# Kernel optimization log

Measured on AMD Instinct MI355X. Metric: run time of the kernel, lower is better.

The kernel has to match this reference:

```python
import jax, jax.numpy as jnp
import numpy as np

EPS = 1e-6
HEADS = 8


def _block_weights(gh, gw):
    # block centers at (i+0.5, j+0.5); 'cos' transform, column-normalized (sum over dim 0)
    ii, jj = np.meshgrid(np.arange(gh) + 0.5, np.arange(gw) + 0.5, indexing='ij')
    centers = np.stack([ii.ravel(), jj.ravel()], axis=-1)  # [N, 2]
    d = np.linalg.norm(centers[:, None, :] - centers[None, :, :], axis=-1)  # [N, N]
    mat = np.cos(d / d.max() * np.pi / 4.0)
    mat = mat / mat.sum(axis=0, keepdims=True)
    return jnp.asarray(mat, dtype=jnp.float32)


def setup_inputs() -> dict:
    key = jax.random.key(0)
    ks = jax.random.split(key, 5)
    B, N, W, C = 8, 256, 49, 512
    s = 1.0 / np.sqrt(C)
    return {
        'x': jax.random.normal(ks[0], (B, N, W, C), jnp.float32),
        'ln_g': jnp.ones((C,), jnp.float32),
        'ln_b': jnp.zeros((C,), jnp.float32),
        'w_qkv': jax.random.normal(ks[1], (3 * C, C), jnp.float32) * s,  # Linear(dim, 3*dim, bias=False)
        'lepe_w': jax.random.normal(ks[2], (C, 1, 5, 5), jnp.float32) * 0.2,  # depthwise 5x5
        'lepe_b': jnp.zeros((C,), jnp.float32),
        'w_out': jax.random.normal(ks[3], (C, C), jnp.float32) * s,
        'b_out': jnp.zeros((C,), jnp.float32),
    }


def reference(x, ln_g, ln_b, w_qkv, lepe_w, lepe_b, w_out, b_out):
    B, N, Wn, C = x.shape
    H = HEADS
    D = C // H
    gh = gw = int(round(N ** 0.5))   # grid of window blocks
    wh = ww = int(round(Wn ** 0.5))  # tokens per window side

    # LayerNorm over channel dim (torch eps=1e-5, biased var)
    mu = x.mean(-1, keepdims=True)
    var = x.var(-1, keepdims=True)
    xn = (x - mu) / jnp.sqrt(var + 1e-5) * ln_g + ln_b

    # qkv projection
    qkv = jnp.einsum('bnwc,oc->bnwo', xn, w_qkv)
    q, k, v = jnp.split(qkv, 3, axis=-1)  # each [B, N, W, C]

    # LePE: fold v to image [B, C, gh*wh, gw*ww], depthwise conv 5x5 pad 2, unfold back
    img = v.reshape(B, gh, gw, wh, ww, C).transpose(0, 5, 1, 3, 2, 4).reshape(B, C, gh * wh, gw * ww)
    lepe = jax.lax.conv_general_dilated(
        img, lepe_w, window_strides=(1, 1), padding=((2, 2), (2, 2)),
        dimension_numbers=('NCHW', 'OIHW', 'NCHW'), feature_group_count=C)
    lepe = lepe + lepe_b[None, :, None, None]
    lepe = lepe.reshape(B, C, gh, wh, gw, ww).transpose(0, 2, 4, 3, 5, 1).reshape(B, N, Wn, C)

    # ReLU + eps feature maps (qk_norm=False -> identity norms)
    q = jax.nn.relu(q) + EPS
    k = jax.nn.relu(k) + EPS

    # split heads: [B, H, N, W, D]
    def split_heads(t):
        return t.reshape(B, N, Wn, H, D).transpose(0, 3, 1, 2, 4)
    q, k, v = split_heads(q), split_heads(k), split_heads(v)

    # per-block k^T v state: [B, H, N, D, D]
    kv = jnp.einsum('bhnwd,bhnwe->bhnde', k, v)
    weight = _block_weights(gh, gw)  # [N, N]
    kv = jnp.einsum('ij,bhjde->bhide', weight, kv)

    k_sum = k.sum(axis=-2)  # [B, H, N, D]
    qk_sum = jnp.einsum('bhnwd,bhnd->bhnw', q, k_sum)[..., None]  # [B, H, N, W, 1]
    normalizer = jnp.einsum('ij,bhjwo->bhiwo', weight, qk_sum) + EPS

    out = jnp.einsum('bhnwd,bhnde->bhnwe', q, kv) / normalizer  # [B, H, N, W, D]
    out = out.transpose(0, 2, 3, 1, 4).reshape(B, N, Wn, C)
    out = out + lepe
    return jnp.einsum('bnwc,oc->bnwo', out, w_out) + b_out
```

## Files before the change

### kernel.cpp

```cpp
#include <hip/hip_runtime.h>
#include <cstdint>

typedef unsigned short u16;
typedef unsigned int   u32;
typedef u16   u16x8 __attribute__((ext_vector_type(8)));
typedef u16   u16x4 __attribute__((ext_vector_type(4)));
typedef float f32x4 __attribute__((ext_vector_type(4)));
typedef __bf16 bf16x8 __attribute__((ext_vector_type(8)));

#define NB    256
#define WTOK  49
#define CH    512
#define HEADS 8
#define DH    64
#define TOK   100352
#define CO    1536

__device__ __forceinline__ u16 f2bf(float f) {
  u32 u = __float_as_uint(f);
  u = (u + 0x7FFFu + ((u >> 16) & 1u)) >> 16;
  return (u16)u;
}
__device__ __forceinline__ float bf2f(u16 u) { return __uint_as_float(((u32)u) << 16); }

__device__ __forceinline__ void load_lds16(const void* g, void* l) {
  __builtin_amdgcn_global_load_lds(
      reinterpret_cast<__attribute__((address_space(1))) void*>(reinterpret_cast<uintptr_t>(g)),
      reinterpret_cast<__attribute__((address_space(3))) void*>(reinterpret_cast<uintptr_t>(l)),
      16, 0, 0);
}

__global__ void cvt_f32_bf16(const float* __restrict__ in, u16* __restrict__ out, int n8) {
  int i = blockIdx.x * 256 + threadIdx.x;
  if (i < n8) {
    f32x4 a = *(const f32x4*)(in + (long)i * 8);
    f32x4 b = *(const f32x4*)(in + (long)i * 8 + 4);
    u16x8 o;
    o[0]=f2bf(a[0]); o[1]=f2bf(a[1]); o[2]=f2bf(a[2]); o[3]=f2bf(a[3]);
    o[4]=f2bf(b[0]); o[5]=f2bf(b[1]); o[6]=f2bf(b[2]); o[7]=f2bf(b[3]);
    *(u16x8*)(out + (long)i * 8) = o;
  }
}

__global__ void prep_wle(const float* __restrict__ lepe_w, float* __restrict__ wle) {
  int i = blockIdx.x * 256 + threadIdx.x;
  if (i < 12800) {
    int c = i / 25, kk = i % 25;
    wle[kk * 512 + c] = lepe_w[i];
  }
}

__global__ void weight_kernel(u16* __restrict__ Wbf, float* __restrict__ Wt) {
  int j = blockIdx.x, i = threadIdx.x;
  float iy = (float)(i >> 4) + 0.5f, ix = (float)(i & 15) + 0.5f;
  float jy = (float)(j >> 4) + 0.5f, jx = (float)(j & 15) + 0.5f;
  float dy = iy - jy, dx = ix - jx;
  float d = sqrtf(dy * dy + dx * dx);
  const float dmax = 21.213203435596427f;
  float m = cosf(d * (0.78539816339744831f / dmax));
  __shared__ float red[256];
  red[i] = m;
  __syncthreads();
  for (int s = 128; s > 0; s >>= 1) {
    if (i < s) red[i] += red[i + s];
    __syncthreads();
  }
  float w = m / red[0];
  Wbf[i * 256 + j] = f2bf(w);
  Wt[j * 256 + i] = w;
}

__global__ __launch_bounds__(256) void ln_kernel(const float* __restrict__ x,
                                                 const float* __restrict__ g,
                                                 const float* __restrict__ bta,
                                                 u16* __restrict__ xn) {
  int wave = threadIdx.x >> 6, lane = threadIdx.x & 63;
  long t = (long)blockIdx.x * 4 + wave;
  const float* xp = x + t * CH + lane * 8;
  f32x4 a = *(const f32x4*)xp;
  f32x4 b = *(const f32x4*)(xp + 4);
  float s  = a[0]+a[1]+a[2]+a[3]+b[0]+b[1]+b[2]+b[3];
  float sq = a[0]*a[0]+a[1]*a[1]+a[2]*a[2]+a[3]*a[3]+b[0]*b[0]+b[1]*b[1]+b[2]*b[2]+b[3]*b[3];
  for (int m = 1; m < 64; m <<= 1) { s += __shfl_xor(s, m); sq += __shfl_xor(sq, m); }
  float mu = s * (1.0f / 512.0f);
  float var = sq * (1.0f / 512.0f) - mu * mu;
  float rstd = rsqrtf(var + 1e-5f);
  const float* gp = g + lane * 8;
  const float* bp = bta + lane * 8;
  f32x4 g0 = *(const f32x4*)gp, g1 = *(const f32x4*)(gp + 4);
  f32x4 b0 = *(const f32x4*)bp, b1 = *(const f32x4*)(bp + 4);
  u16x8 o;
  o[0] = f2bf((a[0]-mu)*rstd*g0[0] + b0[0]);
  o[1] = f2bf((a[1]-mu)*rstd*g0[1] + b0[1]);
  o[2] = f2bf((a[2]-mu)*rstd*g0[2] + b0[2]);
  o[3] = f2bf((a[3]-mu)*rstd*g0[3] + b0[3]);
  o[4] = f2bf((b[0]-mu)*rstd*g1[0] + b1[0]);
  o[5] = f2bf((b[1]-mu)*rstd*g1[1] + b1[1]);
  o[6] = f2bf((b[2]-mu)*rstd*g1[2] + b1[2]);
  o[7] = f2bf((b[3]-mu)*rstd*g1[3] + b1[3]);
  *(u16x8*)(xn + t * CH + lane * 8) = o;
}

template <int KT>
__device__ __forceinline__ void kstepD(char* sm, const u16* sA, const u16* sB,
                                       int t, int lane_off, int wm, int wn,
                                       f32x4 (&acc)[4][4]) {
  if constexpr (KT + 1 < 16) {
    char* d = sm + ((KT + 1) & 1) * 24576 + t * 16;
    load_lds16(sA + (KT + 1) * 32, d);
    load_lds16(sA + 128 * 512 + (KT + 1) * 32, d + 8192);
    load_lds16(sB + (KT + 1) * 32, d + 16384);
  }
  const char* base = sm + (KT & 1) * 24576 + lane_off;
  bf16x8 fa[4], fb[4];
#pragma unroll
  for (int m = 0; m < 4; m++) fa[m] = *(const bf16x8*)(base + (wm * 4 + m) * 1024);
#pragma unroll
  for (int n = 0; n < 4; n++) fb[n] = *(const bf16x8*)(base + 16384 + (wn * 4 + n) * 1024);
  __builtin_amdgcn_s_setprio(1);
#pragma unroll
  for (int m = 0; m < 4; m++)
#pragma unroll
    for (int n = 0; n < 4; n++)
      acc[m][n] = __builtin_amdgcn_mfma_f32_16x16x32_bf16(fa[m], fb[n], acc[m][n], 0, 0, 0);
  __builtin_amdgcn_s_setprio(0);
  if constexpr (KT + 1 < 16) __syncthreads();
}

template <int EPI>
__global__ __launch_bounds__(512, 4)
void gemmD(const u16* __restrict__ A, const u16* __restrict__ B,
           void* __restrict__ C, const float* __restrict__ bias, int N, int nbn) {
  __shared__ __align__(16) char sm[49152];
  const int nwg = gridDim.x, bid = blockIdx.x;
  const int cpx = nwg >> 3;
  const int vid = (bid & 7) * cpx + (bid >> 3);
  const int bn = vid % nbn, bm = vid / nbn;
  const int t = threadIdx.x, lane = t & 63, wave = t >> 6;
  const int wm = wave >> 1, wn = wave & 1;
  const int fr = lane & 15, fq = lane >> 4;
  const int lane_off = (fr >> 1) * 128 + ((((fr & 1) << 2) + fq) ^ (fr >> 1)) * 16;
  const int sl = (t & 7) ^ ((t >> 3) & 7);
  const u16* sA = A + ((long)bm * 256 + ((t >> 3) << 1) + (sl >> 2)) * 512 + (sl & 3) * 8;
  const u16* sB = B + ((long)bn * 128 + ((t >> 3) << 1) + (sl >> 2)) * 512 + (sl & 3) * 8;
  f32x4 acc[4][4] = {};
  {
    char* d = sm + t * 16;
    load_lds16(sA, d);
    load_lds16(sA + 128 * 512, d + 8192);
    load_lds16(sB, d + 16384);
  }
  __syncthreads();
  kstepD<0>(sm, sA, sB, t, lane_off, wm, wn, acc);
  kstepD<1>(sm, sA, sB, t, lane_off, wm, wn, acc);
  kstepD<2>(sm, sA, sB, t, lane_off, wm, wn, acc);
  kstepD<3>(sm, sA, sB, t, lane_off, wm, wn, acc);
  kstepD<4>(sm, sA, sB, t, lane_off, wm, wn, acc);
  kstepD<5>(sm, sA, sB, t, lane_off, wm, wn, acc);
  kstepD<6>(sm, sA, sB, t, lane_off, wm, wn, acc);
  kstepD<7>(sm, sA, sB, t, lane_off, wm, wn, acc);
  kstepD<8>(sm, sA, sB, t, lane_off, wm, wn, acc);
  kstepD<9>(sm, sA, sB, t, lane_off, wm, wn, acc);
  kstepD<10>(sm, sA, sB, t, lane_off, wm, wn, acc);
  kstepD<11>(sm, sA, sB, t, lane_off, wm, wn, acc);
  kstepD<12>(sm, sA, sB, t, lane_off, wm, wn, acc);
  kstepD<13>(sm, sA, sB, t, lane_off, wm, wn, acc);
  kstepD<14>(sm, sA, sB, t, lane_off, wm, wn, acc);
  kstepD<15>(sm, sA, sB, t, lane_off, wm, wn, acc);
  __syncthreads();
  {
    float* ep = (float*)sm + wave * 1088;
    const long r0 = (long)bm * 256 + wm * 64;
    const int c0 = bn * 128 + wn * 64;
    const int rrow = lane >> 2;
    const int cb = (lane & 3) * 16;
#pragma unroll
    for (int m = 0; m < 4; m++) {
#pragma unroll
      for (int n = 0; n < 4; n++) {
        int c = c0 + n * 16 + fr;
        float badd = (EPI == 2) ? bias[c] : 0.0f;
#pragma unroll
        for (int jj = 0; jj < 4; jj++) {
          float v = acc[m][n][jj];
          if (EPI == 1) { if (c < 1024) v = fmaxf(v, 0.0f) + 1e-6f; }
          if (EPI == 2) v += badd;
          ep[(fq * 4 + jj) * 68 + n * 16 + fr] = v;
        }
      }
      f32x4 rr[4];
#pragma unroll
      for (int i = 0; i < 4; i++)
        rr[i] = *(const f32x4*)&ep[rrow * 68 + cb + i * 4];
      long gr = r0 + m * 16 + rrow;
      if (EPI == 2) {
        float* gp = (float*)C + gr * N + c0 + cb;
#pragma unroll
        for (int i = 0; i < 4; i++) *(f32x4*)(gp + i * 4) = rr[i];
      } else {
        u16x8 o0, o1;
#pragma unroll
        for (int i = 0; i < 4; i++) {
          o0[i] = f2bf(rr[0][i]); o0[4 + i] = f2bf(rr[1][i]);
          o1[i] = f2bf(rr[2][i]); o1[4 + i] = f2bf(rr[3][i]);
        }
        u16* gp = (u16*)C + gr * N + c0 + cb;
        *(u16x8*)gp = o0;
        *(u16x8*)(gp + 8) = o1;
      }
    }
  }
}

template <int EPI>
__global__ __launch_bounds__(256)
void gemm_bt(const u16* __restrict__ A, const u16* __restrict__ B,
             void* __restrict__ C, const float* __restrict__ bias,
             int M, int N, int K, long sAb, long sBb, long sCb) {
  __shared__ u16 As[128 * 32];
  __shared__ u16 Bs[128 * 32];
  const int tid = threadIdx.x;
  const int lane = tid & 63;
  const int wave = tid >> 6;
  const int fr = lane & 15, fq = lane >> 4;
  const int wr = (wave >> 1) * 64, wc = (wave & 1) * 64;
  const long bm = blockIdx.y, bn = blockIdx.x, bz = blockIdx.z;
  const u16* Ab = A + bz * sAb + bm * 128 * (long)K;
  const u16* Bb = B + bz * sBb + bn * 128 * (long)K;
  const int srow = tid >> 2;
  const int scol = (tid & 3) * 8;
  f32x4 acc[4][4] = {};
  for (int k0 = 0; k0 < K; k0 += 32) {
    load_lds16(Ab + (long)srow * K + k0 + scol, As + tid * 8);
    load_lds16(Ab + (long)(srow + 64) * K + k0 + scol, As + 2048 + tid * 8);
    load_lds16(Bb + (long)srow * K + k0 + scol, Bs + tid * 8);
    load_lds16(Bb + (long)(srow + 64) * K + k0 + scol, Bs + 2048 + tid * 8);
    __syncthreads();
    bf16x8 af[4], bf[4];
#pragma unroll
    for (int m = 0; m < 4; m++) af[m] = *(const bf16x8*)&As[(wr + m * 16 + fr) * 32 + fq * 8];
#pragma unroll
    for (int n = 0; n < 4; n++) bf[n] = *(const bf16x8*)&Bs[(wc + n * 16 + fr) * 32 + fq * 8];
#pragma unroll
    for (int m = 0; m < 4; m++)
#pragma unroll
      for (int n = 0; n < 4; n++)
        acc[m][n] = __builtin_amdgcn_mfma_f32_16x16x32_bf16(af[m], bf[n], acc[m][n], 0, 0, 0);
    __syncthreads();
  }
#pragma unroll
  for (int m = 0; m < 4; m++) {
    int r0 = wr + m * 16 + fq * 4;
#pragma unroll
    for (int n = 0; n < 4; n++) {
      int c = (int)bn * 128 + wc + n * 16 + fr;
#pragma unroll
      for (int jj = 0; jj < 4; jj++) {
        long r = bm * 128 + r0 + jj;
        float v = acc[m][n][jj];
        if (EPI == 1) { if (c < 1024) v = fmaxf(v, 0.0f) + 1e-6f; }
        if (EPI == 2) {
          ((float*)C)[bz * sCb + r * N + c] = v + bias[c];
        } else {
          ((u16*)C)[bz * sCb + r * N + c] = f2bf(v);
        }
      }
    }
  }
}

__global__ __launch_bounds__(256)
void fold_v(const u16* __restrict__ qkv, u16* __restrict__ vimg) {
  long i = (long)blockIdx.x * 256 + threadIdx.x;
  int tok = (int)(i >> 6);
  int c0 = ((int)i & 63) * 8;
  int w = tok % WTOK, n = tok / WTOK;
  int b = n >> 8, blk = n & 255;
  int gi = blk >> 4, gj = blk & 15;
  int wi = w / 7, wj = w - wi * 7;
  int y = gi * 7 + wi + 2, x = gj * 7 + wj + 2;
  u16x8 v = *(const u16x8*)(qkv + (long)tok * CO + 1024 + c0);
  *(u16x8*)(vimg + (((long)(b * 116 + y)) * 116 + x) * 512 + c0) = v;
}

__global__ __launch_bounds__(256)
void zero_border(u16* __restrict__ vimg) {
  int y = blockIdx.x, b = blockIdx.y;
  int tid = threadIdx.x;
  u16* row = vimg + ((long)(b * 116 + y)) * 116 * 512;
  u16x8 z = {};
  if (y < 2 || y >= 114) {
    for (int i = tid; i < 116 * 512 / 8; i += 256) *(u16x8*)(row + i * 8) = z;
  } else {
    int col = tid >> 6;
    int x = (col < 2) ? col : 112 + col;
    *(u16x8*)(row + x * 512 + (tid & 63) * 8) = z;
  }
}

__global__ __launch_bounds__(256, 2)
void lepe_conv3(const u16* __restrict__ vimg, const float* __restrict__ wle,
                const float* __restrict__ lb, u16* __restrict__ lepe) {
  const int tid = threadIdx.x;
  const int c0 = (tid & 127) * 4;
  const int x  = blockIdx.x * 2 + (tid >> 7);
  const int ys = blockIdx.y * 14;
  const int b  = blockIdx.z;
  f32x4 wv[25];
#pragma unroll
  for (int k = 0; k < 25; k++) wv[k] = *(const f32x4*)(wle + k * 512 + c0);
  const f32x4 bias = *(const f32x4*)(lb + c0);
  const u16* rbase = vimg + (((long)(b * 116 + ys)) * 116 + x) * 512 + c0;
  u16x4 win[5][5];
#pragma unroll
  for (int j = 0; j < 4; j++) {
    const u16* rp = rbase + (long)j * (116 * 512);
#pragma unroll
    for (int kx = 0; kx < 5; kx++) win[j][kx] = *(const u16x4*)(rp + kx * 512);
  }
  const int gj = x / 7, wj = x - gj * 7;
  u16* ob = lepe + (((long)(b * 256 + blockIdx.y * 32 + gj)) * 49 + wj) * 512 + c0;
#pragma unroll
  for (int i = 0; i < 14; i++) {
    {
      const u16* rp = rbase + (long)(i + 4) * (116 * 512);
#pragma unroll
      for (int kx = 0; kx < 5; kx++) win[(i + 4) % 5][kx] = *(const u16x4*)(rp + kx * 512);
    }
    f32x4 acc = bias;
#pragma unroll
    for (int s = 0; s < 5; s++)
#pragma unroll
      for (int kx = 0; kx < 5; kx++) {
        u16x4 v = win[(i + s) % 5][kx];
        f32x4 w = wv[s * 5 + kx];
#pragma unroll
        for (int c = 0; c < 4; c++) acc[c] += bf2f(v[c]) * w[c];
      }
    u16x4 o;
#pragma unroll
    for (int c = 0; c < 4; c++) o[c] = f2bf(acc[c]);
    *(u16x4*)(ob + ((i / 7) * 784 + (i % 7) * 7) * 512) = o;
  }
}

__global__ __launch_bounds__(256)
void kv_local_kernel(const u16* __restrict__ qkv, u16* __restrict__ KVl,
                     float* __restrict__ qk_sum) {
  int n = blockIdx.x, h = blockIdx.y, b = blockIdx.z;
  int bh = b * HEADS + h;
  long tbase = ((long)(b * NB + n)) * WTOK;
  __shared__ u16 kT[64 * 72];
  __shared__ u16 vT[64 * 72];
  __shared__ u16 qs[49 * 72];
  __shared__ float ksum[64];
  __shared__ float qkp[256];
  int tid = threadIdx.x;
  for (int i = tid; i < (64 * 72) / 2; i += 256) {
    ((u32*)kT)[i] = 0;
    ((u32*)vT)[i] = 0;
  }
  __syncthreads();
  {
    int w = tid >> 3, d0 = (tid & 7) * 8;
    u16x8 k8 = *(const u16x8*)(qkv + (tbase + w) * CO + 512 + h * 64 + d0);
    u16x8 v8 = *(const u16x8*)(qkv + (tbase + w) * CO + 1024 + h * 64 + d0);
#pragma unroll
    for (int i = 0; i < 8; i++) { kT[(d0 + i) * 72 + w] = k8[i]; vT[(d0 + i) * 72 + w] = v8[i]; }
    int w2 = w + 32;
    if (w2 < WTOK) {
      u16x8 k82 = *(const u16x8*)(qkv + (tbase + w2) * CO + 512 + h * 64 + d0);
      u16x8 v82 = *(const u16x8*)(qkv + (tbase + w2) * CO + 1024 + h * 64 + d0);
#pragma unroll
      for (int i = 0; i < 8; i++) { kT[(d0 + i) * 72 + w2] = k82[i]; vT[(d0 + i) * 72 + w2] = v82[i]; }
    }
    if (tid < 196) {
      int wq = tid >> 2, dq = (tid & 3) * 16;
      u16x8 q0 = *(const u16x8*)(qkv + (tbase + wq) * CO + h * 64 + dq);
      u16x8 q1 = *(const u16x8*)(qkv + (tbase + wq) * CO + h * 64 + dq + 8);
      *(u16x8*)&qs[wq * 72 + dq] = q0;
      *(u16x8*)&qs[wq * 72 + dq + 8] = q1;
    }
  }
  __syncthreads();
  if (tid < 64) {
    float s = 0.0f;
#pragma unroll
    for (int c = 0; c < 9; c++) {
      u16x8 r = *(const u16x8*)&kT[tid * 72 + c * 8];
#pragma unroll
      for (int i = 0; i < 8; i++) s += bf2f(r[i]);
    }
    ksum[tid] = s;
  }
  __syncthreads();
  if (tid < 196) {
    int w = tid >> 2, d0 = (tid & 3) * 16;
    float s = 0.0f;
#pragma unroll
    for (int i = 0; i < 16; i++) s += bf2f(qs[w * 72 + d0 + i]) * ksum[d0 + i];
    qkp[tid] = s;
  }
  __syncthreads();
  if (tid < WTOK) {
    float s = qkp[tid * 4] + qkp[tid * 4 + 1] + qkp[tid * 4 + 2] + qkp[tid * 4 + 3];
    qk_sum[((long)bh * NB + n) * WTOK + tid] = s;
  }
  int lane = tid & 63, wave = tid >> 6;
  int fr = lane & 15, fq = lane >> 4;
  f32x4 acc[4] = {};
#pragma unroll
  for (int ks = 0; ks < 2; ks++) {
    bf16x8 a = *(const bf16x8*)&kT[(wave * 16 + fr) * 72 + ks * 32 + fq * 8];
#pragma unroll
    for (int n4 = 0; n4 < 4; n4++) {
      bf16x8 bb = *(const bf16x8*)&vT[(n4 * 16 + fr) * 72 + ks * 32 + fq * 8];
      acc[n4] = __builtin_amdgcn_mfma_f32_16x16x32_bf16(a, bb, acc[n4], 0, 0, 0);
    }
  }
  long obase = ((long)bh * NB + n) * 4096;
#pragma unroll
  for (int n4 = 0; n4 < 4; n4++)
#pragma unroll
    for (int jj = 0; jj < 4; jj++) {
      int d = wave * 16 + fq * 4 + jj;
      int e = n4 * 16 + fr;
      KVl[obase + d * 64 + e] = f2bf(acc[n4][jj]);
    }
}

__global__ __launch_bounds__(256)
void transpose_kv(const u16* __restrict__ in, u16* __restrict__ out) {
  int dt = blockIdx.x, jt = blockIdx.y, bh = blockIdx.z;
  __shared__ u16 t[64 * 72];
  int tid = threadIdx.x;
  {
    int jr = tid >> 2, c0 = (tid & 3) * 16;
    const u16* ip = in + ((long)bh * NB + jt * 64 + jr) * 4096 + dt * 64 + c0;
    *(u16x8*)&t[jr * 72 + c0] = *(const u16x8*)ip;
    *(u16x8*)&t[jr * 72 + c0 + 8] = *(const u16x8*)(ip + 8);
  }
  __syncthreads();
  {
    int der = tid >> 2, j0 = (tid & 3) * 16;
    u16x8 o0, o1;
#pragma unroll
    for (int i = 0; i < 8; i++) o0[i] = t[(j0 + i) * 72 + der];
#pragma unroll
    for (int i = 0; i < 8; i++) o1[i] = t[(j0 + 8 + i) * 72 + der];
    u16* op = out + ((long)bh * 4096 + dt * 64 + der) * 256 + jt * 64 + j0;
    *(u16x8*)op = o0;
    *(u16x8*)(op + 8) = o1;
  }
}

__global__ __launch_bounds__(256)
void norm_kernel(const float* __restrict__ Wt, const float* __restrict__ qk_sum,
                 float* __restrict__ inv_norm) {
  int bh = blockIdx.x, tid = threadIdx.x;
  __shared__ float qk[NB * WTOK];
  for (int i = tid; i < NB * WTOK; i += 256) qk[i] = qk_sum[(long)bh * NB * WTOK + i];
  __syncthreads();
  float acc[WTOK];
#pragma unroll
  for (int w = 0; w < WTOK; w++) acc[w] = 0.0f;
  for (int j = 0; j < NB; j++) {
    float wv = Wt[j * NB + tid];
#pragma unroll
    for (int w = 0; w < WTOK; w++) acc[w] += wv * qk[j * WTOK + w];
  }
  long ob = ((long)bh * NB + tid) * WTOK;
#pragma unroll
  for (int w = 0; w < WTOK; w++) inv_norm[ob + w] = 1.0f / (acc[w] + 1e-6f);
}

__global__ __launch_bounds__(256)
void attn_out_kernel(const u16* __restrict__ qkv, const u16* __restrict__ kvm,
                     const float* __restrict__ inv_norm, const u16* __restrict__ lepe,
                     u16* __restrict__ ebuf) {
  int n = blockIdx.x, h = blockIdx.y, b = blockIdx.z;
  int bh = b * HEADS + h;
  long tbase = ((long)(b * NB + n)) * WTOK;
  __shared__ u16 qs[64 * 72];
  __shared__ u16 kvT[64 * 72];
  __shared__ float inv[WTOK];
  int tid = threadIdx.x;
  if (tid < 196) {
    int w = tid >> 2, d0 = (tid & 3) * 16;
    u16x8 q0 = *(const u16x8*)(qkv + (tbase + w) * CO + h * 64 + d0);
    u16x8 q1 = *(const u16x8*)(qkv + (tbase + w) * CO + h * 64 + d0 + 8);
    *(u16x8*)&qs[w * 72 + d0] = q0;
    *(u16x8*)&qs[w * 72 + d0 + 8] = q1;
  }
  {
    int d = tid >> 2, e0 = (tid & 3) * 16;
    const u16* kp = kvm + ((long)bh * NB + n) * 4096 + d * 64 + e0;
    u16x8 k0 = *(const u16x8*)kp;
    u16x8 k1 = *(const u16x8*)(kp + 8);
#pragma unroll
    for (int i = 0; i < 8; i++) { kvT[(e0 + i) * 72 + d] = k0[i]; kvT[(e0 + 8 + i) * 72 + d] = k1[i]; }
  }
  if (tid < WTOK) inv[tid] = inv_norm[((long)bh * NB + n) * WTOK + tid];
  __syncthreads();
  int lane = tid & 63, wave = tid >> 6;
  int fr = lane & 15, fq = lane >> 4;
  f32x4 acc[4] = {};
#pragma unroll
  for (int ks = 0; ks < 2; ks++) {
    bf16x8 a = *(const bf16x8*)&qs[(wave * 16 + fr) * 72 + ks * 32 + fq * 8];
#pragma unroll
    for (int n4 = 0; n4 < 4; n4++) {
      bf16x8 bb = *(const bf16x8*)&kvT[(n4 * 16 + fr) * 72 + ks * 32 + fq * 8];
      acc[n4] = __builtin_amdgcn_mfma_f32_16x16x32_bf16(a, bb, acc[n4], 0, 0, 0);
    }
  }
#pragma unroll
  for (int n4 = 0; n4 < 4; n4++)
#pragma unroll
    for (int jj = 0; jj < 4; jj++) {
      int w = wave * 16 + fq * 4 + jj;
      if (w < WTOK) {
        int e = n4 * 16 + fr;
        long off = (tbase + w) * CH + h * 64 + e;
        float v = acc[n4][jj] * inv[w] + bf2f(lepe[off]);
        ebuf[off] = f2bf(v);
      }
    }
}

static const size_t OFF_XN    = 0;
static const size_t OFF_QKV   = 102760448;
static const size_t OFF_KVL   = OFF_QKV + 308281344;
static const size_t OFF_KVT   = OFF_KVL + 134217728;
static const size_t OFF_QKS   = OFF_KVT + 134217728;
static const size_t OFF_INV   = OFF_QKS + 3211264;
static const size_t OFF_WBF   = OFF_INV + 3211264;
static const size_t OFF_WTF   = OFF_WBF + 131072;
static const size_t OFF_WQKVB = OFF_WTF + 262144;
static const size_t OFF_WOUTB = OFF_WQKVB + 1572864;
static const size_t OFF_WLE   = OFF_WOUTB + 524288;

extern "C" void kernel_launch(void* const* d_in, const int* in_sizes, int n_in,
                              void* d_out, int out_size, void* d_ws, size_t ws_size,
                              hipStream_t stream) {
  const float* x      = (const float*)d_in[0];
  const float* ln_g   = (const float*)d_in[1];
  const float* ln_b   = (const float*)d_in[2];
  const float* w_qkv  = (const float*)d_in[3];
  const float* lepe_w = (const float*)d_in[4];
  const float* lepe_b = (const float*)d_in[5];
  const float* w_out  = (const float*)d_in[6];
  const float* b_out  = (const float*)d_in[7];
  float* out = (float*)d_out;
  char* ws = (char*)d_ws;

  u16*   xn     = (u16*)(ws + OFF_XN);
  u16*   lepe   = (u16*)(ws + OFF_XN);
  u16*   qkv    = (u16*)(ws + OFF_QKV);
  u16*   KVl    = (u16*)(ws + OFF_KVL);
  u16*   kvm    = (u16*)(ws + OFF_KVL);
  u16*   vimg   = (u16*)(ws + OFF_KVT);
  u16*   KVT    = (u16*)(ws + OFF_KVT);
  u16*   ebuf   = (u16*)(ws + OFF_KVT);
  float* qks    = (float*)(ws + OFF_QKS);
  float* invn   = (float*)(ws + OFF_INV);
  u16*   Wbf    = (u16*)(ws + OFF_WBF);
  float* Wt     = (float*)(ws + OFF_WTF);
  u16*   wqkvb  = (u16*)(ws + OFF_WQKVB);
  u16*   woutb  = (u16*)(ws + OFF_WOUTB);
  float* wle    = (float*)(ws + OFF_WLE);

  cvt_f32_bf16<<<384, 256, 0, stream>>>(w_qkv, wqkvb, 98304);
  cvt_f32_bf16<<<128, 256, 0, stream>>>(w_out, woutb, 32768);
  prep_wle<<<50, 256, 0, stream>>>(lepe_w, wle);
  weight_kernel<<<256, 256, 0, stream>>>(Wbf, Wt);
  zero_border<<<dim3(116, 8), 256, 0, stream>>>(vimg);

  ln_kernel<<<25088, 256, 0, stream>>>(x, ln_g, ln_b, xn);

  gemmD<1><<<4704, 512, 0, stream>>>(xn, wqkvb, (void*)qkv, nullptr, CO, 12);

  fold_v<<<25088, 256, 0, stream>>>(qkv, vimg);
  lepe_conv3<<<dim3(56, 8, 8), 256, 0, stream>>>(vimg, wle, lepe_b, lepe);

  kv_local_kernel<<<dim3(NB, HEADS, 8), 256, 0, stream>>>(qkv, KVl, qks);

  transpose_kv<<<dim3(64, 4, 64), 256, 0, stream>>>(KVl, KVT);

  gemm_bt<0><<<dim3(32, 2, 64), 256, 0, stream>>>(Wbf, KVT, (void*)kvm, nullptr,
                                                  NB, 4096, NB,
                                                  0, (long)4096 * 256, (long)256 * 4096);

  norm_kernel<<<64, 256, 0, stream>>>(Wt, qks, invn);

  attn_out_kernel<<<dim3(NB, HEADS, 8), 256, 0, stream>>>(qkv, kvm, invn, lepe, ebuf);

  gemmD<2><<<1568, 512, 0, stream>>>(ebuf, woutb, (void*)out, b_out, CH, 4);
}
```

Measured before the change: 936.2 us.

## Fuse V fold into QKV GEMM epilogue and compute two conv columns per thread

The QKV GEMM epilogue now writes the V columns straight into the padded image layout instead of a full qkv buffer, and the separate fold_v kernel is removed. kv_local reads V from that image, q/k are stored with a 1024 stride, and ebuf moves to a region that no longer overlaps vimg. The depthwise LePE conv now computes two adjacent x outputs per thread, reusing the overlapping window loads with half as many blocks. This removes one full read/write pass over V and some redundant conv loads, at the cost of scattered epilogue stores and more registers in the conv.

Measured after the change: 891.4 us. -4.8%, faster.

```diff
diff --git a/kernel.cpp b/kernel.cpp
--- a/kernel.cpp
+++ b/kernel.cpp
@@ -14,7 +14,6 @@
 #define HEADS 8
 #define DH    64
 #define TOK   100352
-#define CO    1536
 
 __device__ __forceinline__ u16 f2bf(float f) {
   u32 u = __float_as_uint(f);
@@ -130,7 +129,8 @@
 template <int EPI>
 __global__ __launch_bounds__(512, 4)
 void gemmD(const u16* __restrict__ A, const u16* __restrict__ B,
-           void* __restrict__ C, const float* __restrict__ bias, int N, int nbn) {
+           void* __restrict__ C, u16* __restrict__ vimg,
+           const float* __restrict__ bias, int ldc, int nbn) {
   __shared__ __align__(16) char sm[49152];
   const int nwg = gridDim.x, bid = blockIdx.x;
   const int cpx = nwg >> 3;
@@ -174,6 +174,7 @@
     const int c0 = bn * 128 + wn * 64;
     const int rrow = lane >> 2;
     const int cb = (lane & 3) * 16;
+    const int cc = c0 + cb;
 #pragma unroll
     for (int m = 0; m < 4; m++) {
 #pragma unroll
@@ -194,7 +195,7 @@
         rr[i] = *(const f32x4*)&ep[rrow * 68 + cb + i * 4];
       long gr = r0 + m * 16 + rrow;
       if (EPI == 2) {
-        float* gp = (float*)C + gr * N + c0 + cb;
+        float* gp = (float*)C + gr * ldc + cc;
 #pragma unroll
         for (int i = 0; i < 4; i++) *(f32x4*)(gp + i * 4) = rr[i];
       } else {
@@ -204,7 +205,20 @@
           o0[i] = f2bf(rr[0][i]); o0[4 + i] = f2bf(rr[1][i]);
           o1[i] = f2bf(rr[2][i]); o1[4 + i] = f2bf(rr[3][i]);
         }
-        u16* gp = (u16*)C + gr * N + c0 + cb;
+        u16* gp;
+        if (cc < 1024) {
+          gp = (u16*)C + gr * ldc + cc;
+        } else {
+          int tok = (int)gr;
+          int b2 = tok / 12544;
+          int rem = tok - b2 * 12544;
+          int nn = rem / 49;
+          int w = rem - nn * 49;
+          int wi = w / 7, wj = w - wi * 7;
+          int y = (nn >> 4) * 7 + wi + 2;
+          int xx = (nn & 15) * 7 + wj + 2;
+          gp = vimg + (((long)(b2 * 116 + y)) * 116 + xx) * 512 + (cc - 1024);
+        }
         *(u16x8*)gp = o0;
         *(u16x8*)(gp + 8) = o1;
       }
@@ -270,20 +284,6 @@
 }
 
 __global__ __launch_bounds__(256)
-void fold_v(const u16* __restrict__ qkv, u16* __restrict__ vimg) {
-  long i = (long)blockIdx.x * 256 + threadIdx.x;
-  int tok = (int)(i >> 6);
-  int c0 = ((int)i & 63) * 8;
-  int w = tok % WTOK, n = tok / WTOK;
-  int b = n >> 8, blk = n & 255;
-  int gi = blk >> 4, gj = blk & 15;
-  int wi = w / 7, wj = w - wi * 7;
-  int y = gi * 7 + wi + 2, x = gj * 7 + wj + 2;
-  u16x8 v = *(const u16x8*)(qkv + (long)tok * CO + 1024 + c0);
-  *(u16x8*)(vimg + (((long)(b * 116 + y)) * 116 + x) * 512 + c0) = v;
-}
-
-__global__ __launch_bounds__(256)
 void zero_border(u16* __restrict__ vimg) {
   int y = blockIdx.x, b = blockIdx.y;
   int tid = threadIdx.x;
@@ -299,57 +299,66 @@
 }
 
 __global__ __launch_bounds__(256, 2)
-void lepe_conv3(const u16* __restrict__ vimg, const float* __restrict__ wle,
+void lepe_conv4(const u16* __restrict__ vimg, const float* __restrict__ wle,
                 const float* __restrict__ lb, u16* __restrict__ lepe) {
   const int tid = threadIdx.x;
   const int c0 = (tid & 127) * 4;
-  const int x  = blockIdx.x * 2 + (tid >> 7);
+  const int x0 = blockIdx.x * 4 + (tid >> 7) * 2;
   const int ys = blockIdx.y * 14;
   const int b  = blockIdx.z;
   f32x4 wv[25];
 #pragma unroll
   for (int k = 0; k < 25; k++) wv[k] = *(const f32x4*)(wle + k * 512 + c0);
   const f32x4 bias = *(const f32x4*)(lb + c0);
-  const u16* rbase = vimg + (((long)(b * 116 + ys)) * 116 + x) * 512 + c0;
-  u16x4 win[5][5];
+  const u16* rbase = vimg + (((long)(b * 116 + ys)) * 116 + x0) * 512 + c0;
+  u16x4 win[5][6];
 #pragma unroll
   for (int j = 0; j < 4; j++) {
     const u16* rp = rbase + (long)j * (116 * 512);
 #pragma unroll
-    for (int kx = 0; kx < 5; kx++) win[j][kx] = *(const u16x4*)(rp + kx * 512);
-  }
-  const int gj = x / 7, wj = x - gj * 7;
-  u16* ob = lepe + (((long)(b * 256 + blockIdx.y * 32 + gj)) * 49 + wj) * 512 + c0;
+    for (int kx = 0; kx < 6; kx++) win[j][kx] = *(const u16x4*)(rp + kx * 512);
+  }
+  const int gj0 = x0 / 7, wj0 = x0 - gj0 * 7;
+  const int gj1 = (x0 + 1) / 7, wj1 = (x0 + 1) - gj1 * 7;
+  u16* ob0 = lepe + (((long)(b * 256 + blockIdx.y * 32 + gj0)) * 49 + wj0) * 512 + c0;
+  u16* ob1 = lepe + (((long)(b * 256 + blockIdx.y * 32 + gj1)) * 49 + wj1) * 512 + c0;
 #pragma unroll
   for (int i = 0; i < 14; i++) {
     {
       const u16* rp = rbase + (long)(i + 4) * (116 * 512);
 #pragma unroll
-      for (int kx = 0; kx < 5; kx++) win[(i + 4) % 5][kx] = *(const u16x4*)(rp + kx * 512);
-    }
-    f32x4 acc = bias;
+      for (int kx = 0; kx < 6; kx++) win[(i + 4) % 5][kx] = *(const u16x4*)(rp + kx * 512);
+    }
+    f32x4 a0 = bias, a1 = bias;
 #pragma unroll
     for (int s = 0; s < 5; s++)
 #pragma unroll
       for (int kx = 0; kx < 5; kx++) {
-        u16x4 v = win[(i + s) % 5][kx];
+        u16x4 v0 = win[(i + s) % 5][kx];
+        u16x4 v1 = win[(i + s) % 5][kx + 1];
         f32x4 w = wv[s * 5 + kx];
 #pragma unroll
-        for (int c = 0; c < 4; c++) acc[c] += bf2f(v[c]) * w[c];
+        for (int c = 0; c < 4; c++) {
+          a0[c] += bf2f(v0[c]) * w[c];
+          a1[c] += bf2f(v1[c]) * w[c];
+        }
       }
-    u16x4 o;
-#pragma unroll
-    for (int c = 0; c < 4; c++) o[c] = f2bf(acc[c]);
-    *(u16x4*)(ob + ((i / 7) * 784 + (i % 7) * 7) * 512) = o;
+    u16x4 o0, o1;
+#pragma unroll
+    for (int c = 0; c < 4; c++) { o0[c] = f2bf(a0[c]); o1[c] = f2bf(a1[c]); }
+    long so = (long)((i / 7) * 784 + (i % 7) * 7) * 512;
+    *(u16x4*)(ob0 + so) = o0;
+    *(u16x4*)(ob1 + so) = o1;
   }
 }
 
 __global__ __launch_bounds__(256)
-void kv_local_kernel(const u16* __restrict__ qkv, u16* __restrict__ KVl,
-                     float* __restrict__ qk_sum) {
+void kv_local_kernel(const u16* __restrict__ qk, const u16* __restrict__ vimg,
+                     u16* __restrict__ KVl, float* __restrict__ qk_sum) {
   int n = blockIdx.x, h = blockIdx.y, b = blockIdx.z;
   int bh = b * HEADS + h;
   long tbase = ((long)(b * NB + n)) * WTOK;
+  const int gi = n >> 4, gj = n & 15;
   __shared__ u16 kT[64 * 72];
   __shared__ u16 vT[64 * 72];
   __shared__ u16 qs[49 * 72];
@@ -363,21 +372,25 @@
   __syncthreads();
   {
     int w = tid >> 3, d0 = (tid & 7) * 8;
-    u16x8 k8 = *(const u16x8*)(qkv + (tbase + w) * CO + 512 + h * 64 + d0);
-    u16x8 v8 = *(const u16x8*)(qkv + (tbase + w) * CO + 1024 + h * 64 + d0);
+    u16x8 k8 = *(const u16x8*)(qk + (tbase + w) * 1024 + 512 + h * 64 + d0);
+    int wi = w / 7, wj = w - wi * 7;
+    long va = (((long)(b * 116 + gi * 7 + wi + 2)) * 116 + (gj * 7 + wj + 2)) * 512 + h * 64 + d0;
+    u16x8 v8 = *(const u16x8*)(vimg + va);
 #pragma unroll
     for (int i = 0; i < 8; i++) { kT[(d0 + i) * 72 + w] = k8[i]; vT[(d0 + i) * 72 + w] = v8[i]; }
     int w2 = w + 32;
     if (w2 < WTOK) {
-      u16x8 k82 = *(const u16x8*)(qkv + (tbase + w2) * CO + 512 + h * 64 + d0);
-      u16x8 v82 = *(const u16x8*)(qkv + (tbase + w2) * CO + 1024 + h * 64 + d0);
+      u16x8 k82 = *(const u16x8*)(qk + (tbase + w2) * 1024 + 512 + h * 64 + d0);
+      int wi2 = w2 / 7, wj2 = w2 - wi2 * 7;
+      long va2 = (((long)(b * 116 + gi * 7 + wi2 + 2)) * 116 + (gj * 7 + wj2 + 2)) * 512 + h * 64 + d0;
+      u16x8 v82 = *(const u16x8*)(vimg + va2);
 #pragma unroll
       for (int i = 0; i < 8; i++) { kT[(d0 + i) * 72 + w2] = k82[i]; vT[(d0 + i) * 72 + w2] = v82[i]; }
     }
     if (tid < 196) {
       int wq = tid >> 2, dq = (tid & 3) * 16;
-      u16x8 q0 = *(const u16x8*)(qkv + (tbase + wq) * CO + h * 64 + dq);
-      u16x8 q1 = *(const u16x8*)(qkv + (tbase + wq) * CO + h * 64 + dq + 8);
+      u16x8 q0 = *(const u16x8*)(qk + (tbase + wq) * 1024 + h * 64 + dq);
+      u16x8 q1 = *(const u16x8*)(qk + (tbase + wq) * 1024 + h * 64 + dq + 8);
       *(u16x8*)&qs[wq * 72 + dq] = q0;
       *(u16x8*)&qs[wq * 72 + dq + 8] = q1;
     }
@@ -475,7 +488,7 @@
 }
 
 __global__ __launch_bounds__(256)
-void attn_out_kernel(const u16* __restrict__ qkv, const u16* __restrict__ kvm,
+void attn_out_kernel(const u16* __restrict__ qk, const u16* __restrict__ kvm,
                      const float* __restrict__ inv_norm, const u16* __restrict__ lepe,
                      u16* __restrict__ ebuf) {
   int n = blockIdx.x, h = blockIdx.y, b = blockIdx.z;
@@ -487,8 +500,8 @@
   int tid = threadIdx.x;
   if (tid < 196) {
     int w = tid >> 2, d0 = (tid & 3) * 16;
-    u16x8 q0 = *(const u16x8*)(qkv + (tbase + w) * CO + h * 64 + d0);
-    u16x8 q1 = *(const u16x8*)(qkv + (tbase + w) * CO + h * 64 + d0 + 8);
+    u16x8 q0 = *(const u16x8*)(qk + (tbase + w) * 1024 + h * 64 + d0);
+    u16x8 q1 = *(const u16x8*)(qk + (tbase + w) * 1024 + h * 64 + d0 + 8);
     *(u16x8*)&qs[w * 72 + d0] = q0;
     *(u16x8*)&qs[w * 72 + d0 + 8] = q1;
   }
@@ -530,6 +543,7 @@
 
 static const size_t OFF_XN    = 0;
 static const size_t OFF_QKV   = 102760448;
+static const size_t OFF_EBUF  = OFF_QKV + 205520896;
 static const size_t OFF_KVL   = OFF_QKV + 308281344;
 static const size_t OFF_KVT   = OFF_KVL + 134217728;
 static const size_t OFF_QKS   = OFF_KVT + 134217728;
@@ -556,12 +570,12 @@
 
   u16*   xn     = (u16*)(ws + OFF_XN);
   u16*   lepe   = (u16*)(ws + OFF_XN);
-  u16*   qkv    = (u16*)(ws + OFF_QKV);
+  u16*   qk     = (u16*)(ws + OFF_QKV);
+  u16*   ebuf   = (u16*)(ws + OFF_EBUF);
   u16*   KVl    = (u16*)(ws + OFF_KVL);
   u16*   kvm    = (u16*)(ws + OFF_KVL);
   u16*   vimg   = (u16*)(ws + OFF_KVT);
   u16*   KVT    = (u16*)(ws + OFF_KVT);
-  u16*   ebuf   = (u16*)(ws + OFF_KVT);
   float* qks    = (float*)(ws + OFF_QKS);
   float* invn   = (float*)(ws + OFF_INV);
   u16*   Wbf    = (u16*)(ws + OFF_WBF);
@@ -578,12 +592,11 @@
 
   ln_kernel<<<25088, 256, 0, stream>>>(x, ln_g, ln_b, xn);
 
-  gemmD<1><<<4704, 512, 0, stream>>>(xn, wqkvb, (void*)qkv, nullptr, CO, 12);
-
-  fold_v<<<25088, 256, 0, stream>>>(qkv, vimg);
-  lepe_conv3<<<dim3(56, 8, 8), 256, 0, stream>>>(vimg, wle, lepe_b, lepe);
-
-  kv_local_kernel<<<dim3(NB, HEADS, 8), 256, 0, stream>>>(qkv, KVl, qks);
+  gemmD<1><<<4704, 512, 0, stream>>>(xn, wqkvb, (void*)qk, vimg, nullptr, 1024, 12);
+
+  lepe_conv4<<<dim3(28, 8, 8), 256, 0, stream>>>(vimg, wle, lepe_b, lepe);
+
+  kv_local_kernel<<<dim3(NB, HEADS, 8), 256, 0, stream>>>(qk, vimg, KVl, qks);
 
   transpose_kv<<<dim3(64, 4, 64), 256, 0, stream>>>(KVl, KVT);
 
@@ -593,7 +606,7 @@
 
   norm_kernel<<<64, 256, 0, stream>>>(Wt, qks, invn);
 
-  attn_out_kernel<<<dim3(NB, HEADS, 8), 256, 0, stream>>>(qkv, kvm, invn, lepe, ebuf);
-
-  gemmD<2><<<1568, 512, 0, stream>>>(ebuf, woutb, (void*)out, b_out, CH, 4);
-}
+  attn_out_kernel<<<dim3(NB, HEADS, 8), 256, 0, stream>>>(qk, kvm, invn, lepe, ebuf);
+
+  gemmD<2><<<1568, 512, 0, stream>>>(ebuf, woutb, (void*)out, nullptr, b_out, 512, 4);
+}
```
